# Kernel optimization log

Measured on AMD Instinct MI355X. Metric: run time of the kernel, lower is better.

The kernel has to match this reference:

```python
import jax, jax.numpy as jnp
import numpy as np

N_HEAD = 16


def setup_inputs() -> dict:
    key = jax.random.key(0)
    ks = jax.random.split(key, 6)
    b, l, d = 4, 2048, 1024
    n_mem = 1000  # FAISS index is populated with 1000 random vectors per batch element
    return {
        "q": jax.random.normal(ks[0], (b, l, d), dtype=jnp.float32),
        "kv": jax.random.normal(ks[1], (b, l, d), dtype=jnp.float32),  # unused by forward (faithful)
        "mem_table": jax.random.uniform(ks[2], (b, n_mem, d), dtype=jnp.float32),
        "w_q": jax.random.normal(ks[3], (d, d), dtype=jnp.float32) / np.sqrt(d),
        "w_kv": jax.random.normal(ks[4], (d, 2 * (d // N_HEAD)), dtype=jnp.float32) / np.sqrt(d),
        "w_concat": jax.random.normal(ks[5], (d, d), dtype=jnp.float32) / np.sqrt(d),
        "topk": 1,
    }


def reference(q, kv, mem_table, w_q, w_kv, w_concat, topk):
    b, l, d = q.shape
    h = N_HEAD
    dh = d // h

    qp = q @ w_q  # (b, l, d)

    # Exact inner-product kNN (topk=1) replacing the per-batch FAISS HNSW search:
    # brute-force scores + argmax + gather of the nearest memory vector.
    knn_scores = jnp.einsum("bld,bnd->bln", qp, mem_table)  # (b, l, n_mem)
    idx = jnp.argmax(knn_scores, axis=-1)  # (b, l) int
    mem = jnp.take_along_axis(mem_table, idx[..., None], axis=1)  # (b, l, d)

    k, v = jnp.split(mem @ w_kv, 2, axis=-1)  # each (b, l, dh)

    qh = qp.reshape(b, l, h, dh).transpose(0, 2, 1, 3)  # (b, h, l, dh)
    # k, v are shared across heads (unsqueeze(1) in torch -> broadcast here)
    att = jnp.einsum("bhld,bmd->bhlm", qh, k) / np.float32(np.sqrt(dh))  # (b, h, l, l)
    att = jax.nn.softmax(att, axis=-1)
    out = jnp.einsum("bhlm,bmd->bhld", att, v)  # (b, h, l, dh)

    out = out.transpose(0, 2, 1, 3).reshape(b, l, d)
    return out @ w_concat
```

## Files before the change

kernel.cpp:

```cpp
#include <hip/hip_runtime.h>
#include <float.h>
#include <math.h>

#define BATCH 4
#define SEQ   2048
#define DIM   1024
#define NHEAD 16
#define DHEAD 64
#define NMEM  1000
#define NPAD  1024
#define ROWS  (BATCH*SEQ)
#define QSCALE 0.18033688011112042f
#define RESCORE_DELTA 0.10f

typedef __attribute__((ext_vector_type(8))) __bf16 bf16x8;
typedef __attribute__((ext_vector_type(4))) __bf16 bf16x4;
typedef __attribute__((ext_vector_type(4))) float  f32x4;

static __device__ inline f32x4 mfma16(bf16x8 a, bf16x8 b, f32x4 c) {
  return __builtin_amdgcn_mfma_f32_16x16x32_bf16(a, b, c, 0, 0, 0);
}

#define GLOAD16(g, l) __builtin_amdgcn_global_load_lds( \
    (const __attribute__((address_space(1))) unsigned int*)(g), \
    (__attribute__((address_space(3))) unsigned int*)(l), 16, 0, 0)

enum { MODE_C = 0, MODE_HILO = 1, MODE_ARGMAX = 2, MODE_KV = 3 };

template<int AF32, int NPROD, int MODE>
__global__ __launch_bounds__(256) void gemm3(
    const void* __restrict__ Ah_, const __bf16* __restrict__ Al,
    const __bf16* __restrict__ Bh, const __bf16* __restrict__ Bl,
    int rowsPerZ, long bStrideZ,
    float* __restrict__ C, __bf16* __restrict__ Oh, __bf16* __restrict__ Ol,
    float* __restrict__ pv, int* __restrict__ pi)
{
  extern __shared__ char smem[];
  const int t = threadIdx.x;
  const int w = t >> 6, lane = t & 63, l15 = lane & 15, g = lane >> 4;
  const int wr = w >> 1, wc = w & 1;
  const int m0 = blockIdx.z * rowsPerZ + blockIdx.x * 128;
  const int n0 = blockIdx.y * 128;
  const __bf16* Bh_b = Bh + (size_t)blockIdx.z * bStrideZ;
  const __bf16* Bl_b = (NPROD == 3) ? (Bl + (size_t)blockIdx.z * bStrideZ) : (const __bf16*)0;

  constexpr int SB = (AF32 || NPROD == 3) ? 32768 : 16384;
  constexpr int BOFF = AF32 ? 16384 : (NPROD == 3 ? 16384 : 8192);

  f32x4 acc[4][4];
  #pragma unroll
  for (int i = 0; i < 4; ++i)
    #pragma unroll
    for (int j = 0; j < 4; ++j) acc[i][j] = (f32x4){0.f, 0.f, 0.f, 0.f};

  auto STAGE = [&](int buf, int k0) {
    char* base = smem + buf * SB;
    if (AF32) {
      const float* Af = (const float*)Ah_;
      #pragma unroll
      for (int i = 0; i < 4; ++i) {
        int c = i * 256 + t;
        int r = c >> 3, s = c & 7;
        int sl = s ^ (r & 7);
        GLOAD16(&Af[(size_t)(m0 + r) * DIM + k0 + sl * 4], base + i * 4096 + w * 1024);
      }
    } else {
      const __bf16* Ab = (const __bf16*)Ah_;
      #pragma unroll
      for (int i = 0; i < 2; ++i) {
        int c = i * 256 + t;
        int r = c >> 2, s = c & 3;
        int sl = s ^ (r & 3);
        GLOAD16(&Ab[(size_t)(m0 + r) * DIM + k0 + sl * 8], base + i * 4096 + w * 1024);
        if (NPROD == 3)
          GLOAD16(&Al[(size_t)(m0 + r) * DIM + k0 + sl * 8], base + 8192 + i * 4096 + w * 1024);
      }
    }
    char* bB = base + BOFF;
    #pragma unroll
    for (int i = 0; i < 2; ++i) {
      int c = i * 256 + t;
      int r = c >> 2, s = c & 3;
      int sl = s ^ (r & 3);
      GLOAD16(&Bh_b[(size_t)(n0 + r) * DIM + k0 + sl * 8], bB + i * 4096 + w * 1024);
      if (NPROD == 3)
        GLOAD16(&Bl_b[(size_t)(n0 + r) * DIM + k0 + sl * 8], bB + 8192 + i * 4096 + w * 1024);
    }
  };

  STAGE(0, 0);
  __syncthreads();
  int cur = 0;

  for (int k0 = 0; k0 < DIM; k0 += 32) {
    if (k0 + 32 < DIM) STAGE(cur ^ 1, k0 + 32);

    char* base = smem + cur * SB;
    char* sA   = base;
    char* sAl  = base + 8192;
    char* sBh  = base + BOFF;
    char* sBl  = sBh + 8192;

    bf16x8 ah[4], al[4], bh[4], bl[4];
    #pragma unroll
    for (int mi = 0; mi < 4; ++mi) {
      int r = wr * 64 + mi * 16 + l15;
      if (AF32) {
        int p0 = (2 * g) ^ (r & 7), p1 = (2 * g + 1) ^ (r & 7);
        float4 q0 = *(const float4*)(sA + r * 128 + p0 * 16);
        float4 q1 = *(const float4*)(sA + r * 128 + p1 * 16);
        float qq[8] = {q0.x, q0.y, q0.z, q0.w, q1.x, q1.y, q1.z, q1.w};
        #pragma unroll
        for (int j = 0; j < 8; ++j) {
          __bf16 h = (__bf16)qq[j];
          ah[mi][j] = h;
          al[mi][j] = (__bf16)(qq[j] - (float)h);
        }
      } else {
        int p = (g ^ (r & 3)) * 16;
        ah[mi] = *(const bf16x8*)(sA + r * 64 + p);
        if (NPROD == 3) al[mi] = *(const bf16x8*)(sAl + r * 64 + p);
      }
    }
    #pragma unroll
    for (int ni = 0; ni < 4; ++ni) {
      int r = wc * 64 + ni * 16 + l15;
      int p = (g ^ (r & 3)) * 16;
      bh[ni] = *(const bf16x8*)(sBh + r * 64 + p);
      if (NPROD == 3) bl[ni] = *(const bf16x8*)(sBl + r * 64 + p);
    }
    __builtin_amdgcn_s_setprio(1);
    #pragma unroll
    for (int mi = 0; mi < 4; ++mi)
      #pragma unroll
      for (int ni = 0; ni < 4; ++ni) {
        acc[mi][ni] = mfma16(ah[mi], bh[ni], acc[mi][ni]);
        if (NPROD == 3) {
          acc[mi][ni] = mfma16(ah[mi], bl[ni], acc[mi][ni]);
          acc[mi][ni] = mfma16(al[mi], bh[ni], acc[mi][ni]);
        }
      }
    __builtin_amdgcn_s_setprio(0);
    __syncthreads();
    cur ^= 1;
  }

  if (MODE == MODE_C) {
    #pragma unroll
    for (int mi = 0; mi < 4; ++mi)
      #pragma unroll
      for (int ni = 0; ni < 4; ++ni) {
        int col = n0 + wc * 64 + ni * 16 + l15;
        #pragma unroll
        for (int r = 0; r < 4; ++r) {
          int row = m0 + wr * 64 + mi * 16 + g * 4 + r;
          C[(size_t)row * DIM + col] = acc[mi][ni][r];
        }
      }
  } else if (MODE == MODE_HILO) {
    #pragma unroll
    for (int mi = 0; mi < 4; ++mi)
      #pragma unroll
      for (int ni = 0; ni < 4; ++ni) {
        int col = n0 + wc * 64 + ni * 16 + l15;
        #pragma unroll
        for (int r = 0; r < 4; ++r) {
          int row = m0 + wr * 64 + mi * 16 + g * 4 + r;
          float v = acc[mi][ni][r] * QSCALE;
          __bf16 h = (__bf16)v;
          Oh[(size_t)row * DIM + col] = h;
          Ol[(size_t)row * DIM + col] = (__bf16)(v - (float)h);
        }
      }
  } else if (MODE == MODE_KV) {
    #pragma unroll
    for (int mi = 0; mi < 4; ++mi)
      #pragma unroll
      for (int ni = 0; ni < 4; ++ni) {
        int col = wc * 64 + ni * 16 + l15;
        #pragma unroll
        for (int r = 0; r < 4; ++r) {
          int gr = m0 + wr * 64 + mi * 16 + g * 4 + r;
          int bb = gr >> 10, n = gr & (NPAD - 1);
          __bf16 h = (__bf16)acc[mi][ni][r];
          if (col < DHEAD) {
            Oh[(size_t)gr * DHEAD + col] = h;
          } else {
            int np = (n & ~63) | ((n & 15) << 2) | ((n >> 4) & 3);
            Ol[((size_t)bb * DHEAD + (col - DHEAD)) * NPAD + np] = h;
          }
        }
      }
  } else {
    #pragma unroll
    for (int mi = 0; mi < 4; ++mi)
      #pragma unroll
      for (int r = 0; r < 4; ++r) {
        float v1 = -FLT_MAX, v2 = -FLT_MAX;
        int   i1 = 0x7fffffff, i2 = 0x7fffffff;
        #pragma unroll
        for (int ni = 0; ni < 4; ++ni) {
          int col = n0 + wc * 64 + ni * 16 + l15;
          float s = (col < NMEM) ? acc[mi][ni][r] : -FLT_MAX;
          if (s > v1 || (s == v1 && col < i1)) { v2 = v1; i2 = i1; v1 = s; i1 = col; }
          else if (s > v2 || (s == v2 && col < i2)) { v2 = s; i2 = col; }
        }
        #pragma unroll
        for (int off = 1; off < 16; off <<= 1) {
          float w1 = __shfl_xor(v1, off), w2 = __shfl_xor(v2, off);
          int   j1 = __shfl_xor(i1, off), j2 = __shfl_xor(i2, off);
          if (w1 > v1 || (w1 == v1 && j1 < i1)) { v2 = v1; i2 = i1; v1 = w1; i1 = j1; }
          else if (w1 > v2 || (w1 == v2 && j1 < i2)) { v2 = w1; i2 = j1; }
          if (w2 > v1 || (w2 == v1 && j2 < i1)) { v2 = v1; i2 = i1; v1 = w2; i1 = j2; }
          else if (w2 > v2 || (w2 == v2 && j2 < i2)) { v2 = w2; i2 = j2; }
        }
        if (l15 == 0) {
          int row = m0 + wr * 64 + mi * 16 + g * 4 + r;
          int half = blockIdx.y * 2 + wc;
          pv[(size_t)(half * 2 + 0) * ROWS + row] = v1;
          pv[(size_t)(half * 2 + 1) * ROWS + row] = v2;
          pi[(size_t)(half * 2 + 0) * ROWS + row] = i1;
          pi[(size_t)(half * 2 + 1) * ROWS + row] = i2;
        }
      }
  }
}

__global__ __launch_bounds__(256) void knn_rescore(const __bf16* __restrict__ qph,
                                                   const __bf16* __restrict__ qpl,
                                                   const float* __restrict__ mem,
                                                   const float* __restrict__ pv,
                                                   const int* __restrict__ pi,
                                                   int* __restrict__ idx) {
  const int t = threadIdx.x;
  const int wq = t >> 6, lane = t & 63;
  const int qrow = blockIdx.x * 4 + wq;
  const int batch = qrow >> 11;

  float cv = (lane < 32) ? pv[(size_t)lane * ROWS + qrow] : -FLT_MAX;
  int   ci = (lane < 32) ? pi[(size_t)lane * ROWS + qrow] : 0x7fffffff;

  float M = cv;
  #pragma unroll
  for (int off = 1; off < 64; off <<= 1) M = fmaxf(M, __shfl_xor(M, off));

  unsigned long long cand = __ballot(cv >= M - RESCORE_DELTA && ci < NMEM);

  float qp[16];
  {
    const __bf16* ph = qph + (size_t)qrow * DIM + lane * 16;
    const __bf16* pl = qpl + (size_t)qrow * DIM + lane * 16;
    #pragma unroll
    for (int j = 0; j < 16; ++j) qp[j] = (float)ph[j] + (float)pl[j];
  }

  float best = -FLT_MAX;
  int besti = 0x7fffffff;
  while (cand) {
    int b = __ffsll((long long)cand) - 1;
    cand &= cand - 1;
    int c = __shfl(ci, b);
    const float* mrow = mem + ((size_t)batch * NMEM + c) * DIM + lane * 16;
    float part = 0.f;
    #pragma unroll
    for (int j = 0; j < 16; ++j) part = fmaf(qp[j], mrow[j], part);
    #pragma unroll
    for (int off = 1; off < 64; off <<= 1) part += __shfl_xor(part, off);
    if (part > best || (part == best && c < besti)) { best = part; besti = c; }
  }
  if (lane == 0) idx[qrow] = besti;
}

__global__ __launch_bounds__(256) void hist_lc(const int* __restrict__ idx,
                                               float* __restrict__ lc) {
  __shared__ int hcnt[NPAD];
  const int t = threadIdx.x, b = blockIdx.x;
  #pragma unroll
  for (int i = 0; i < 4; ++i) hcnt[t + 256 * i] = 0;
  __syncthreads();
  #pragma unroll
  for (int i = 0; i < 8; ++i) atomicAdd(&hcnt[idx[b * SEQ + i * 256 + t]], 1);
  __syncthreads();
  #pragma unroll
  for (int i = 0; i < 4; ++i) {
    int n = t + 256 * i;
    int c = hcnt[n];
    lc[b * NPAD + n] = (n < NMEM && c > 0) ? log2f((float)c) : -1e30f;
  }
}

__global__ __launch_bounds__(256, 2) void attn_table(const __bf16* __restrict__ qph,
                                                     const __bf16* __restrict__ Ktab,
                                                     const __bf16* __restrict__ VtTp,
                                                     const float* __restrict__ lc2,
                                                     __bf16* __restrict__ attn_bf) {
  extern __shared__ char smem[];
  char* sK = smem;
  char* sV = smem + 16384;
  char* sP = smem + 32768;

  const int t = threadIdx.x;
  const int wq = t >> 6, lane = t & 63, l15 = lane & 15, g = lane >> 4;
  const int b = blockIdx.z, h0 = blockIdx.y * 2;
  const int q0 = blockIdx.x * 128 + wq * 32;

  bf16x8 qa[2][2][2];
  #pragma unroll
  for (int hh = 0; hh < 2; ++hh)
    #pragma unroll
    for (int mi = 0; mi < 2; ++mi)
      #pragma unroll
      for (int ks = 0; ks < 2; ++ks)
        qa[hh][mi][ks] = *(const bf16x8*)&qph[(size_t)(b * SEQ + q0 + mi * 16 + l15) * DIM +
                                              (h0 + hh) * DHEAD + ks * 32 + g * 8];

  f32x4 O[2][2][4];
  #pragma unroll
  for (int hh = 0; hh < 2; ++hh)
    #pragma unroll
    for (int mi = 0; mi < 2; ++mi)
      #pragma unroll
      for (int fd = 0; fd < 4; ++fd) O[hh][mi][fd] = (f32x4){0.f, 0.f, 0.f, 0.f};
  float lsum[2][2][4];
  #pragma unroll
  for (int hh = 0; hh < 2; ++hh)
    #pragma unroll
    for (int mi = 0; mi < 2; ++mi)
      #pragma unroll
      for (int r = 0; r < 4; ++r) lsum[hh][mi][r] = 0.f;

  const __bf16* Kb = Ktab + (size_t)b * NPAD * DHEAD;
  const __bf16* Vb = VtTp + (size_t)b * DHEAD * NPAD;
  const float* lcb = lc2 + b * NPAD;
  char* sPw = sP + wq * 4096;

  auto STAGE = [&](int buf, int tile) {
    const int n0 = tile * 64;
    #pragma unroll
    for (int i = 0; i < 2; ++i) {
      int c = i * 256 + t, row = c >> 3, s = c & 7, sl = s ^ (row & 7);
      GLOAD16(&Kb[(size_t)(n0 + row) * DHEAD + sl * 8], sK + buf * 8192 + i * 4096 + wq * 1024);
      GLOAD16(&Vb[(size_t)row * NPAD + n0 + sl * 8], sV + buf * 8192 + i * 4096 + wq * 1024);
    }
  };

  STAGE(0, 0);
  __syncthreads();
  int cur = 0;

  for (int tile = 0; tile < NPAD / 64; ++tile) {
    if (tile + 1 < NPAD / 64) STAGE(cur ^ 1, tile + 1);

    const int n0 = tile * 64;
    float lcv[4];
    #pragma unroll
    for (int ni = 0; ni < 4; ++ni) lcv[ni] = lcb[n0 + ni * 16 + l15];

    bf16x8 kf[2][4];
    #pragma unroll
    for (int ks = 0; ks < 2; ++ks)
      #pragma unroll
      for (int ni = 0; ni < 4; ++ni)
        kf[ks][ni] = *(const bf16x8*)(sK + cur * 8192 + (ni * 16 + l15) * 128 +
                                      (((ks * 4 + g) ^ (l15 & 7)) * 16));

    #pragma unroll
    for (int hh = 0; hh < 2; ++hh) {
      #pragma unroll
      for (int mi = 0; mi < 2; ++mi) {
        f32x4 S[4];
        #pragma unroll
        for (int ni = 0; ni < 4; ++ni) S[ni] = (f32x4){0.f, 0.f, 0.f, 0.f};
        __builtin_amdgcn_s_setprio(1);
        #pragma unroll
        for (int ks = 0; ks < 2; ++ks)
          #pragma unroll
          for (int ni = 0; ni < 4; ++ni)
            S[ni] = mfma16(qa[hh][mi][ks], kf[ks][ni], S[ni]);
        __builtin_amdgcn_s_setprio(0);
        #pragma unroll
        for (int r = 0; r < 4; ++r) {
          int row = mi * 16 + g * 4 + r;
          bf16x4 p4;
          float rs = 0.f;
          #pragma unroll
          for (int ni = 0; ni < 4; ++ni) {
            float p = __builtin_amdgcn_exp2f(S[ni][r] + lcv[ni]);
            rs += p;
            p4[ni] = (__bf16)p;
          }
          *(bf16x4*)(sPw + row * 128 + ((l15 * 8) ^ ((row & 7) << 4))) = p4;
          lsum[hh][mi][r] += rs;
        }
      }
      #pragma unroll
      for (int ks = 0; ks < 2; ++ks) {
        bf16x8 vf[4];
        #pragma unroll
        for (int fd = 0; fd < 4; ++fd)
          vf[fd] = *(const bf16x8*)(sV + cur * 8192 + (fd * 16 + l15) * 128 +
                                    (((ks * 4 + g) ^ (l15 & 7)) * 16));
        __builtin_amdgcn_s_setprio(1);
        #pragma unroll
        for (int mi = 0; mi < 2; ++mi) {
          int row = mi * 16 + l15;
          bf16x8 pa = *(const bf16x8*)(sPw + row * 128 +
                                       ((ks * 64 + g * 16) ^ ((row & 7) << 4)));
          #pragma unroll
          for (int fd = 0; fd < 4; ++fd)
            O[hh][mi][fd] = mfma16(pa, vf[fd], O[hh][mi][fd]);
        }
        __builtin_amdgcn_s_setprio(0);
      }
    }

    __syncthreads();
    cur ^= 1;
  }

  #pragma unroll
  for (int hh = 0; hh < 2; ++hh)
    #pragma unroll
    for (int mi = 0; mi < 2; ++mi)
      #pragma unroll
      for (int r = 0; r < 4; ++r) {
        float rs = lsum[hh][mi][r];
        #pragma unroll
        for (int off = 1; off < 16; off <<= 1) rs += __shfl_xor(rs, off);
        float inv = 1.f / rs;
        size_t row = (size_t)(b * SEQ + q0 + mi * 16 + g * 4 + r);
        #pragma unroll
        for (int fd = 0; fd < 4; ++fd)
          attn_bf[row * DIM + (h0 + hh) * DHEAD + fd * 16 + l15] =
              (__bf16)(O[hh][mi][fd][r] * inv);
      }
}

__global__ __launch_bounds__(256) void cast_weights(const float* __restrict__ w_q,
                                                    const float* __restrict__ w_concat,
                                                    const float* __restrict__ w_kv,
                                                    __bf16* __restrict__ wqt_h,
                                                    __bf16* __restrict__ wqt_l,
                                                    __bf16* __restrict__ wct,
                                                    __bf16* __restrict__ wkvT_h,
                                                    __bf16* __restrict__ wkvT_l) {
  __shared__ float tile[64][65];
  const int t = threadIdx.x;
  const int id = blockIdx.x;
  const float* src;
  __bf16 *oh, *ol;
  int kt, nt, srcStride, writeLo;
  if (id < 256)      { src = w_q;      oh = wqt_h;  ol = wqt_l;  kt = id & 15;         nt = id >> 4;         srcStride = DIM; writeLo = 1; }
  else if (id < 512) { src = w_concat; oh = wct;    ol = 0;      kt = (id - 256) & 15; nt = (id - 256) >> 4; srcStride = DIM; writeLo = 0; }
  else               { src = w_kv;     oh = wkvT_h; ol = wkvT_l; kt = (id - 512) & 15; nt = (id - 512) >> 4; srcStride = 128; writeLo = 1; }
  const int k0 = kt * 64, n0 = nt * 64;
  #pragma unroll
  for (int i = 0; i < 16; ++i) {
    int e = t + i * 256, r = e >> 6, c = e & 63;
    tile[r][c] = src[(size_t)(k0 + r) * srcStride + n0 + c];
  }
  __syncthreads();
  #pragma unroll
  for (int i = 0; i < 16; ++i) {
    int e = t + i * 256, r = e >> 6, c = e & 63;
    float v = tile[c][r];
    __bf16 h = (__bf16)v;
    oh[(size_t)(n0 + r) * DIM + k0 + c] = h;
    if (writeLo) ol[(size_t)(n0 + r) * DIM + k0 + c] = (__bf16)(v - (float)h);
  }
}

__global__ __launch_bounds__(256) void cast_inputs(const float* __restrict__ mem,
                                                   const float* __restrict__ q,
                                                   __bf16* __restrict__ mh,
                                                   __bf16* __restrict__ ml,
                                                   __bf16* __restrict__ qh,
                                                   __bf16* __restrict__ ql) {
  const int id = blockIdx.x;
  if (id < 2048) {
    size_t e = ((size_t)id * 256 + threadIdx.x) * 8;
    int d = (int)(e & 1023);
    size_t rn = e >> 10;
    int n = (int)(rn & 1023), b = (int)(rn >> 10);
    bf16x8 h8, l8;
    if (n < NMEM) {
      const float* p = mem + ((size_t)b * NMEM + n) * DIM + d;
      #pragma unroll
      for (int j = 0; j < 8; ++j) {
        float v = p[j];
        __bf16 h = (__bf16)v;
        h8[j] = h; l8[j] = (__bf16)(v - (float)h);
      }
    } else {
      #pragma unroll
      for (int j = 0; j < 8; ++j) { h8[j] = (__bf16)0.f; l8[j] = (__bf16)0.f; }
    }
    *(bf16x8*)(mh + e) = h8;
    *(bf16x8*)(ml + e) = l8;
  } else {
    size_t e = ((size_t)(id - 2048) * 256 + threadIdx.x) * 8;
    float4 a = *(const float4*)(q + e);
    float4 bq = *(const float4*)(q + e + 4);
    float vv[8] = {a.x, a.y, a.z, a.w, bq.x, bq.y, bq.z, bq.w};
    bf16x8 h8, l8;
    #pragma unroll
    for (int j = 0; j < 8; ++j) {
      __bf16 h = (__bf16)vv[j];
      h8[j] = h; l8[j] = (__bf16)(vv[j] - (float)h);
    }
    *(bf16x8*)(qh + e) = h8;
    *(bf16x8*)(ql + e) = l8;
  }
}

extern "C" void kernel_launch(void* const* d_in, const int* in_sizes, int n_in,
                              void* d_out, int out_size, void* d_ws, size_t ws_size,
                              hipStream_t stream) {
  const float* q        = (const float*)d_in[0];
  const float* mem      = (const float*)d_in[2];
  const float* w_q      = (const float*)d_in[3];
  const float* w_kv     = (const float*)d_in[4];
  const float* w_concat = (const float*)d_in[5];
  float* out = (float*)d_out;

  char* wsb = (char*)d_ws;
  __bf16* memh   = (__bf16*)(wsb + 0);
  __bf16* meml   = (__bf16*)(wsb + 8388608);
  __bf16* wqt_h  = (__bf16*)(wsb + 16777216);
  __bf16* wqt_l  = (__bf16*)(wsb + 18874368);
  __bf16* wct    = (__bf16*)(wsb + 20971520);
  __bf16* Ktab   = (__bf16*)(wsb + 23068672);
  __bf16* VtT    = (__bf16*)(wsb + 23592960);
  float*  lc     = (float*) (wsb + 24117248);
  float*  pv     = (float*) (wsb + 24133632);
  int*    pi     = (int*)   (wsb + 25182208);
  int*    idx    = (int*)   (wsb + 26230784);
  __bf16* wkvT_h = (__bf16*)(wsb + 26263552);
  __bf16* wkvT_l = (__bf16*)(wsb + 26525696);
  __bf16* qph    = (__bf16*)(wsb + 26787840);
  __bf16* qpl    = (__bf16*)(wsb + 43565056);
  __bf16* attn_bf = qpl;
  __bf16* qh = (__bf16*)d_out;
  __bf16* ql = (__bf16*)d_out + (size_t)ROWS * DIM;

  cast_weights<<<dim3(544), 256, 0, stream>>>(w_q, w_concat, w_kv,
                                              wqt_h, wqt_l, wct, wkvT_h, wkvT_l);
  cast_inputs<<<dim3(6144), 256, 0, stream>>>(mem, q, memh, meml, qh, ql);

  gemm3<0, 3, MODE_HILO><<<dim3(64, 8, 1), 256, 65536, stream>>>(
      (const void*)qh, ql, wqt_h, wqt_l, 0, 0,
      (float*)0, qph, qpl, (float*)0, (int*)0);

  gemm3<0, 3, MODE_KV><<<dim3(BATCH * NPAD / 128, 1, 1), 256, 65536, stream>>>(
      (const void*)memh, meml, wkvT_h, wkvT_l, 0, 0,
      (float*)0, Ktab, VtT, (float*)0, (int*)0);

  gemm3<0, 1, MODE_ARGMAX><<<dim3(16, 8, 4), 256, 32768, stream>>>(
      (const void*)qph, (const __bf16*)0, memh, (const __bf16*)0, 2048, (long)NPAD * DIM,
      (float*)0, (__bf16*)0, (__bf16*)0, pv, pi);

  knn_rescore<<<dim3(ROWS / 4), 256, 0, stream>>>(qph, qpl, mem, pv, pi, idx);

  hist_lc<<<dim3(BATCH), 256, 0, stream>>>(idx, lc);

  attn_table<<<dim3(SEQ / 128, NHEAD / 2, BATCH), 256, 49152, stream>>>(
      qph, Ktab, VtT, lc, attn_bf);

  gemm3<0, 1, MODE_C><<<dim3(64, 8, 1), 256, 32768, stream>>>(
      (const void*)attn_bf, (const __bf16*)0, wct, (const __bf16*)0, 0, 0,
      out, (__bf16*)0, (__bf16*)0, (float*)0, (int*)0);
}
```

Measured before the change: 230.9 us.

## Reassociate kNN scoring as q·(mem·Wqᵀ) and drop split-precision Q projection

After: 238.3 us. 3.2% more time.

```diff
diff --git a/kernel.cpp b/kernel.cpp
--- a/kernel.cpp
+++ b/kernel.cpp
@@ -11,7 +11,7 @@
 #define NPAD  1024
 #define ROWS  (BATCH*SEQ)
 #define QSCALE 0.18033688011112042f
-#define RESCORE_DELTA 0.10f
+#define RESCORE_DELTA 0.45f
 
 typedef __attribute__((ext_vector_type(8))) __bf16 bf16x8;
 typedef __attribute__((ext_vector_type(4))) __bf16 bf16x4;
@@ -25,7 +25,7 @@
     (const __attribute__((address_space(1))) unsigned int*)(g), \
     (__attribute__((address_space(3))) unsigned int*)(l), 16, 0, 0)
 
-enum { MODE_C = 0, MODE_HILO = 1, MODE_ARGMAX = 2, MODE_KV = 3 };
+enum { MODE_C = 0, MODE_H = 1, MODE_ARGMAX = 2, MODE_KV = 3, MODE_ZF = 4 };
 
 template<int AF32, int NPROD, int MODE>
 __global__ __launch_bounds__(256) void gemm3(
@@ -55,16 +55,7 @@
 
   auto STAGE = [&](int buf, int k0) {
     char* base = smem + buf * SB;
-    if (AF32) {
-      const float* Af = (const float*)Ah_;
-      #pragma unroll
-      for (int i = 0; i < 4; ++i) {
-        int c = i * 256 + t;
-        int r = c >> 3, s = c & 7;
-        int sl = s ^ (r & 7);
-        GLOAD16(&Af[(size_t)(m0 + r) * DIM + k0 + sl * 4], base + i * 4096 + w * 1024);
-      }
-    } else {
+    {
       const __bf16* Ab = (const __bf16*)Ah_;
       #pragma unroll
       for (int i = 0; i < 2; ++i) {
@@ -105,22 +96,9 @@
     #pragma unroll
     for (int mi = 0; mi < 4; ++mi) {
       int r = wr * 64 + mi * 16 + l15;
-      if (AF32) {
-        int p0 = (2 * g) ^ (r & 7), p1 = (2 * g + 1) ^ (r & 7);
-        float4 q0 = *(const float4*)(sA + r * 128 + p0 * 16);
-        float4 q1 = *(const float4*)(sA + r * 128 + p1 * 16);
-        float qq[8] = {q0.x, q0.y, q0.z, q0.w, q1.x, q1.y, q1.z, q1.w};
-        #pragma unroll
-        for (int j = 0; j < 8; ++j) {
-          __bf16 h = (__bf16)qq[j];
-          ah[mi][j] = h;
-          al[mi][j] = (__bf16)(qq[j] - (float)h);
-        }
-      } else {
-        int p = (g ^ (r & 3)) * 16;
-        ah[mi] = *(const bf16x8*)(sA + r * 64 + p);
-        if (NPROD == 3) al[mi] = *(const bf16x8*)(sAl + r * 64 + p);
-      }
+      int p = (g ^ (r & 3)) * 16;
+      ah[mi] = *(const bf16x8*)(sA + r * 64 + p);
+      if (NPROD == 3) al[mi] = *(const bf16x8*)(sAl + r * 64 + p);
     }
     #pragma unroll
     for (int ni = 0; ni < 4; ++ni) {
@@ -157,7 +135,7 @@
           C[(size_t)row * DIM + col] = acc[mi][ni][r];
         }
       }
-  } else if (MODE == MODE_HILO) {
+  } else if (MODE == MODE_H) {
     #pragma unroll
     for (int mi = 0; mi < 4; ++mi)
       #pragma unroll
@@ -166,10 +144,21 @@
         #pragma unroll
         for (int r = 0; r < 4; ++r) {
           int row = m0 + wr * 64 + mi * 16 + g * 4 + r;
-          float v = acc[mi][ni][r] * QSCALE;
-          __bf16 h = (__bf16)v;
-          Oh[(size_t)row * DIM + col] = h;
-          Ol[(size_t)row * DIM + col] = (__bf16)(v - (float)h);
+          Oh[(size_t)row * DIM + col] = (__bf16)(acc[mi][ni][r] * QSCALE);
+        }
+      }
+  } else if (MODE == MODE_ZF) {
+    #pragma unroll
+    for (int mi = 0; mi < 4; ++mi)
+      #pragma unroll
+      for (int ni = 0; ni < 4; ++ni) {
+        int col = n0 + wc * 64 + ni * 16 + l15;
+        #pragma unroll
+        for (int r = 0; r < 4; ++r) {
+          int row = m0 + wr * 64 + mi * 16 + g * 4 + r;
+          float v = acc[mi][ni][r];
+          C[(size_t)row * DIM + col]  = v;
+          Oh[(size_t)row * DIM + col] = (__bf16)v;
         }
       }
   } else if (MODE == MODE_KV) {
@@ -226,9 +215,8 @@
   }
 }
 
-__global__ __launch_bounds__(256) void knn_rescore(const __bf16* __restrict__ qph,
-                                                   const __bf16* __restrict__ qpl,
-                                                   const float* __restrict__ mem,
+__global__ __launch_bounds__(256) void knn_rescore(const float* __restrict__ qf,
+                                                   const float* __restrict__ Zf,
                                                    const float* __restrict__ pv,
                                                    const int* __restrict__ pi,
                                                    int* __restrict__ idx) {
@@ -246,12 +234,11 @@
 
   unsigned long long cand = __ballot(cv >= M - RESCORE_DELTA && ci < NMEM);
 
-  float qp[16];
+  float qv[16];
   {
-    const __bf16* ph = qph + (size_t)qrow * DIM + lane * 16;
-    const __bf16* pl = qpl + (size_t)qrow * DIM + lane * 16;
-    #pragma unroll
-    for (int j = 0; j < 16; ++j) qp[j] = (float)ph[j] + (float)pl[j];
+    const float* p = qf + (size_t)qrow * DIM + lane * 16;
+    #pragma unroll
+    for (int j = 0; j < 16; ++j) qv[j] = p[j];
   }
 
   float best = -FLT_MAX;
@@ -260,10 +247,10 @@
     int b = __ffsll((long long)cand) - 1;
     cand &= cand - 1;
     int c = __shfl(ci, b);
-    const float* mrow = mem + ((size_t)batch * NMEM + c) * DIM + lane * 16;
+    const float* zrow = Zf + ((size_t)batch * NPAD + c) * DIM + lane * 16;
     float part = 0.f;
     #pragma unroll
-    for (int j = 0; j < 16; ++j) part = fmaf(qp[j], mrow[j], part);
+    for (int j = 0; j < 16; ++j) part = fmaf(qv[j], zrow[j], part);
     #pragma unroll
     for (int off = 1; off < 64; off <<= 1) part += __shfl_xor(part, off);
     if (part > best || (part == best && c < besti)) { best = part; besti = c; }
@@ -440,7 +427,8 @@
                                                     const float* __restrict__ w_concat,
                                                     const float* __restrict__ w_kv,
                                                     __bf16* __restrict__ wqt_h,
-                                                    __bf16* __restrict__ wqt_l,
+                                                    __bf16* __restrict__ wqn_h,
+                                                    __bf16* __restrict__ wqn_l,
                                                     __bf16* __restrict__ wct,
                                                     __bf16* __restrict__ wkvT_h,
                                                     __bf16* __restrict__ wkvT_l) {
@@ -450,14 +438,20 @@
   const float* src;
   __bf16 *oh, *ol;
   int kt, nt, srcStride, writeLo;
-  if (id < 256)      { src = w_q;      oh = wqt_h;  ol = wqt_l;  kt = id & 15;         nt = id >> 4;         srcStride = DIM; writeLo = 1; }
+  if (id < 256)      { src = w_q;      oh = wqt_h;  ol = 0;      kt = id & 15;         nt = id >> 4;         srcStride = DIM; writeLo = 0; }
   else if (id < 512) { src = w_concat; oh = wct;    ol = 0;      kt = (id - 256) & 15; nt = (id - 256) >> 4; srcStride = DIM; writeLo = 0; }
   else               { src = w_kv;     oh = wkvT_h; ol = wkvT_l; kt = (id - 512) & 15; nt = (id - 512) >> 4; srcStride = 128; writeLo = 1; }
   const int k0 = kt * 64, n0 = nt * 64;
   #pragma unroll
   for (int i = 0; i < 16; ++i) {
     int e = t + i * 256, r = e >> 6, c = e & 63;
-    tile[r][c] = src[(size_t)(k0 + r) * srcStride + n0 + c];
+    float v = src[(size_t)(k0 + r) * srcStride + n0 + c];
+    tile[r][c] = v;
+    if (id < 256) {
+      __bf16 h = (__bf16)v;
+      wqn_h[(size_t)(k0 + r) * DIM + n0 + c] = h;
+      wqn_l[(size_t)(k0 + r) * DIM + n0 + c] = (__bf16)(v - (float)h);
+    }
   }
   __syncthreads();
   #pragma unroll
@@ -474,8 +468,7 @@
                                                    const float* __restrict__ q,
                                                    __bf16* __restrict__ mh,
                                                    __bf16* __restrict__ ml,
-                                                   __bf16* __restrict__ qh,
-                                                   __bf16* __restrict__ ql) {
+                                                   __bf16* __restrict__ qh) {
   const int id = blockIdx.x;
   if (id < 2048) {
     size_t e = ((size_t)id * 256 + threadIdx.x) * 8;
@@ -502,14 +495,10 @@
     float4 a = *(const float4*)(q + e);
     float4 bq = *(const float4*)(q + e + 4);
     float vv[8] = {a.x, a.y, a.z, a.w, bq.x, bq.y, bq.z, bq.w};
-    bf16x8 h8, l8;
-    #pragma unroll
-    for (int j = 0; j < 8; ++j) {
-      __bf16 h = (__bf16)vv[j];
-      h8[j] = h; l8[j] = (__bf16)(vv[j] - (float)h);
-    }
+    bf16x8 h8;
+    #pragma unroll
+    for (int j = 0; j < 8; ++j) h8[j] = (__bf16)vv[j];
     *(bf16x8*)(qh + e) = h8;
-    *(bf16x8*)(ql + e) = l8;
   }
 }
 
@@ -527,39 +516,44 @@
   __bf16* memh   = (__bf16*)(wsb + 0);
   __bf16* meml   = (__bf16*)(wsb + 8388608);
   __bf16* wqt_h  = (__bf16*)(wsb + 16777216);
-  __bf16* wqt_l  = (__bf16*)(wsb + 18874368);
-  __bf16* wct    = (__bf16*)(wsb + 20971520);
-  __bf16* Ktab   = (__bf16*)(wsb + 23068672);
-  __bf16* VtT    = (__bf16*)(wsb + 23592960);
-  float*  lc     = (float*) (wsb + 24117248);
-  float*  pv     = (float*) (wsb + 24133632);
-  int*    pi     = (int*)   (wsb + 25182208);
-  int*    idx    = (int*)   (wsb + 26230784);
-  __bf16* wkvT_h = (__bf16*)(wsb + 26263552);
-  __bf16* wkvT_l = (__bf16*)(wsb + 26525696);
-  __bf16* qph    = (__bf16*)(wsb + 26787840);
-  __bf16* qpl    = (__bf16*)(wsb + 43565056);
-  __bf16* attn_bf = qpl;
+  __bf16* wqn_h  = (__bf16*)(wsb + 18874368);
+  __bf16* wqn_l  = (__bf16*)(wsb + 20971520);
+  __bf16* wct    = (__bf16*)(wsb + 23068672);
+  __bf16* Ktab   = (__bf16*)(wsb + 25165824);
+  __bf16* VtT    = (__bf16*)(wsb + 25690112);
+  float*  lc     = (float*) (wsb + 26214400);
+  float*  pv     = (float*) (wsb + 26230784);
+  int*    pi     = (int*)   (wsb + 27279360);
+  int*    idx    = (int*)   (wsb + 28327936);
+  __bf16* wkvT_h = (__bf16*)(wsb + 28360704);
+  __bf16* wkvT_l = (__bf16*)(wsb + 28622848);
+  __bf16* qph    = (__bf16*)(wsb + 28884992);
+  float*  Zf     = (float*) (wsb + 45662208);
+  __bf16* Zh     = (__bf16*)(wsb + 62439424);
+  __bf16* attn_bf = (__bf16*)Zf;
   __bf16* qh = (__bf16*)d_out;
-  __bf16* ql = (__bf16*)d_out + (size_t)ROWS * DIM;
 
   cast_weights<<<dim3(544), 256, 0, stream>>>(w_q, w_concat, w_kv,
-                                              wqt_h, wqt_l, wct, wkvT_h, wkvT_l);
-  cast_inputs<<<dim3(6144), 256, 0, stream>>>(mem, q, memh, meml, qh, ql);
-
-  gemm3<0, 3, MODE_HILO><<<dim3(64, 8, 1), 256, 65536, stream>>>(
-      (const void*)qh, ql, wqt_h, wqt_l, 0, 0,
-      (float*)0, qph, qpl, (float*)0, (int*)0);
+                                              wqt_h, wqn_h, wqn_l, wct, wkvT_h, wkvT_l);
+  cast_inputs<<<dim3(6144), 256, 0, stream>>>(mem, q, memh, meml, qh);
+
+  gemm3<0, 3, MODE_ZF><<<dim3(BATCH * NPAD / 128, 8, 1), 256, 65536, stream>>>(
+      (const void*)memh, meml, wqn_h, wqn_l, 0, 0,
+      Zf, Zh, (__bf16*)0, (float*)0, (int*)0);
 
   gemm3<0, 3, MODE_KV><<<dim3(BATCH * NPAD / 128, 1, 1), 256, 65536, stream>>>(
       (const void*)memh, meml, wkvT_h, wkvT_l, 0, 0,
       (float*)0, Ktab, VtT, (float*)0, (int*)0);
 
+  gemm3<0, 1, MODE_H><<<dim3(64, 8, 1), 256, 32768, stream>>>(
+      (const void*)qh, (const __bf16*)0, wqt_h, (const __bf16*)0, 0, 0,
+      (float*)0, qph, (__bf16*)0, (float*)0, (int*)0);
+
   gemm3<0, 1, MODE_ARGMAX><<<dim3(16, 8, 4), 256, 32768, stream>>>(
-      (const void*)qph, (const __bf16*)0, memh, (const __bf16*)0, 2048, (long)NPAD * DIM,
+      (const void*)qh, (const __bf16*)0, Zh, (const __bf16*)0, 2048, (long)NPAD * DIM,
       (float*)0, (__bf16*)0, (__bf16*)0, pv, pi);
 
-  knn_rescore<<<dim3(ROWS / 4), 256, 0, stream>>>(qph, qpl, mem, pv, pi, idx);
+  knn_rescore<<<dim3(ROWS / 4), 256, 0, stream>>>(q, Zf, pv, pi, idx);
 
   hist_lc<<<dim3(BATCH), 256, 0, stream>>>(idx, lc);
 
```
